# Kernel tuning notes

Measured on AMD Instinct MI355X. Metric: run time of the kernel, lower is better.

Reference implementation:

```python
import jax, jax.numpy as jnp
import numpy as np

K = 9  # kernel_size (knn neighbors, loop=True -> self included)

def setup_inputs() -> dict:
    key = jax.random.key(0)
    k1, k2, k3 = jax.random.split(key, 3)
    B, C, H, W = 8, 64, 32, 32
    OUT = 64
    x = jax.random.normal(k1, (B, C, H, W), dtype=jnp.float32)
    # SAGEConv params: lin_l (neighbor aggregate, with bias), lin_r (root, no bias)
    s = 1.0 / np.sqrt(C)
    W_l = jax.random.uniform(k2, (OUT, C), minval=-s, maxval=s, dtype=jnp.float32)
    b_l = jnp.zeros((OUT,), dtype=jnp.float32)
    W_r = jax.random.uniform(k3, (OUT, C), minval=-s, maxval=s, dtype=jnp.float32)
    return {"x": x, "W_l": W_l, "b_l": b_l, "W_r": W_r}

def _knn_mean(x_f, batches):
    # squared-euclidean pairwise distances [N, N], masked across batches
    sq = jnp.sum(x_f * x_f, axis=-1)
    dist = sq[:, None] + sq[None, :] - 2.0 * (x_f @ x_f.T)
    cross = batches[:, None] != batches[None, :]
    dist = jnp.where(cross, jnp.inf, dist)
    neg, idx = jax.lax.top_k(-dist, K)          # k nearest (self included, dist 0)
    valid = (neg != -jnp.inf).astype(x_f.dtype)  # handle degenerate last-batch node
    nbr = x_f[idx] * valid[..., None]            # [N, K, C]
    return nbr.sum(axis=1) / valid.sum(axis=1, keepdims=True)

def reference(x, W_l, b_l, W_r):
    B, C, H, Wd = x.shape
    N = B * H * Wd
    x_f = x.transpose(0, 2, 3, 1).reshape(N, C)  # flat_nodes: [B*H*W, C]
    # torch.linspace(0, B, steps=N).to(int64): truncation of i*B/(N-1)
    batches = jnp.linspace(0.0, float(B), N).astype(jnp.int32)
    mean_nbr = _knn_mean(x_f, batches)
    # SAGEConv: lin_l(mean_j x_j) + lin_r(x_i)
    return mean_nbr @ W_l.T + b_l + x_f @ W_r.T
```

## Files before the change

kernel.cpp:

```cpp
#include <hip/hip_runtime.h>
#include <cstdint>
#include <cstddef>


__global__ __launch_bounds__(256, 2) void k_dist(const float* __restrict__ x,
                                                 const float* __restrict__ Wl,
                                                 const float* __restrict__ Wr,
                                                 const float* __restrict__ bl,
                                                 float* __restrict__ yl,
                                                 float* __restrict__ yr,
                                                 float* __restrict__ D) {
  __shared__ float4 SH[2112];
  float4* As4 = SH;
  float4* Bs4 = SH + 1056;
  __shared__ float sqA[128];
  __shared__ float sqB[128];
  int bi = (int)blockIdx.x;
  int t = threadIdx.x;
  int tx = t & 15, ty = t >> 4;

  bool is_w = (bi >= 288);
  int i0, j0 = 0, sb = 0, ti = 0, tj = 0;
  if (is_w) {
    i0 = (bi - 288) << 7;
  } else {
    int b = bi / 36;
    int rem = bi - b * 36;
    while (rem >= 8 - ti) { rem -= (8 - ti); ++ti; }
    tj = ti + rem;
    sb = b << 10;
    i0 = sb + (ti << 7);
    j0 = sb + (tj << 7);
  }
  const float* xA = x + (((size_t)(i0 >> 10)) << 16) + (i0 & 1023);
  const float* xB = is_w ? xA : x + (((size_t)(j0 >> 10)) << 16) + (j0 & 1023);

  float acc[8][8];
#pragma unroll
  for (int r = 0; r < 8; ++r)
#pragma unroll
    for (int c = 0; c < 8; ++c) acc[r][c] = 0.f;

#pragma unroll 1
  for (int pass = 0; pass < 2; ++pass) {
    if (pass) __syncthreads();
    int c0 = pass << 5;
#pragma unroll
    for (int i = 0; i < 4; ++i) {
      int u = t + (i << 8);
      int c = u >> 5, m4 = u & 31;
      As4[c * 33 + m4] = *(const float4*)&xA[((size_t)(c0 + c) << 10) + (m4 << 2)];
    }
    if (!is_w) {
#pragma unroll
      for (int i = 0; i < 4; ++i) {
        int u = t + (i << 8);
        int c = u >> 5, m4 = u & 31;
        Bs4[c * 33 + m4] = *(const float4*)&xB[((size_t)(c0 + c) << 10) + (m4 << 2)];
      }
    } else {
#pragma unroll
      for (int i = 0; i < 16; ++i) {
        int u = t + (i << 8);
        int j = u >> 5, c = u & 31;
        const float* Wsrc = (j < 64) ? Wl : Wr;
        int jr = j & 63;
        ((float*)&Bs4[c * 33 + (j >> 2)])[j & 3] = Wsrc[(jr << 6) + c0 + c];
      }
    }
    __syncthreads();
    if (!is_w) {
      int m = t & 127;
      const float* base = (t < 128) ? (const float*)As4 : (const float*)Bs4;
      float p = 0.f;
#pragma unroll
      for (int c = 0; c < 32; ++c) {
        float v = base[(c * 33 + (m >> 2)) * 4 + (m & 3)];
        p = fmaf(v, v, p);
      }
      float* dst = (t < 128) ? sqA : sqB;
      if (pass == 0) dst[m] = p; else dst[m] += p;
    }
#pragma unroll 4
    for (int k = 0; k < 32; ++k) {
      float4 a0 = As4[k * 33 + ty];
      float4 a1 = As4[k * 33 + 16 + ty];
      float4 b0 = Bs4[k * 33 + tx];
      float4 b1 = Bs4[k * 33 + 16 + tx];
      float av[8] = {a0.x, a0.y, a0.z, a0.w, a1.x, a1.y, a1.z, a1.w};
      float bv[8] = {b0.x, b0.y, b0.z, b0.w, b1.x, b1.y, b1.z, b1.w};
#pragma unroll
      for (int r = 0; r < 8; ++r)
#pragma unroll
        for (int c = 0; c < 8; ++c)
          acc[r][c] = fmaf(av[r], bv[c], acc[r][c]);
    }
  }
  __syncthreads();

  int rloc[8];
#pragma unroll
  for (int r = 0; r < 4; ++r) { rloc[r] = (ty << 2) + r; rloc[4 + r] = 64 + (ty << 2) + r; }

  if (is_w) {
    float4 blv = *(const float4*)&bl[tx << 2];
#pragma unroll
    for (int r = 0; r < 8; ++r) {
      int n = i0 + rloc[r];
      float4 o0, o1;
      o0.x = acc[r][0]; o0.y = acc[r][1]; o0.z = acc[r][2]; o0.w = acc[r][3];
      o1.x = acc[r][4] + blv.x; o1.y = acc[r][5] + blv.y;
      o1.z = acc[r][6] + blv.z; o1.w = acc[r][7] + blv.w;
      *(float4*)&yl[((size_t)n << 6) + (tx << 2)] = o0;
      *(float4*)&yr[((size_t)n << 6) + (tx << 2)] = o1;
    }
    return;
  }

  int cloc[8];
#pragma unroll
  for (int c = 0; c < 4; ++c) { cloc[c] = (tx << 2) + c; cloc[4 + c] = 64 + (tx << 2) + c; }
  float sqi[8], sqj[8];
#pragma unroll
  for (int r = 0; r < 8; ++r) sqi[r] = sqA[rloc[r]];
#pragma unroll
  for (int c = 0; c < 8; ++c) sqj[c] = sqB[cloc[c]];
#pragma unroll
  for (int r = 0; r < 8; ++r)
#pragma unroll
    for (int c = 0; c < 8; ++c)
      acc[r][c] = sqi[r] + sqj[c] - 2.f * acc[r][c];
#pragma unroll
  for (int r = 0; r < 8; ++r) {
    size_t rb = ((size_t)(i0 + rloc[r]) << 10) + (j0 - sb);
    float4 o0, o1;
    o0.x = acc[r][0]; o0.y = acc[r][1]; o0.z = acc[r][2]; o0.w = acc[r][3];
    o1.x = acc[r][4]; o1.y = acc[r][5]; o1.z = acc[r][6]; o1.w = acc[r][7];
    *(float4*)&D[rb + (tx << 2)] = o0;
    *(float4*)&D[rb + 64 + (tx << 2)] = o1;
  }
  if (ti != tj) {
    float* tb = (float*)SH;
#pragma unroll 1
    for (int h = 0; h < 2; ++h) {
      __syncthreads();
#pragma unroll
      for (int r = 0; r < 8; ++r)
#pragma unroll
        for (int c = 0; c < 4; ++c)
          tb[((tx << 2) + c) * 132 + rloc[r]] = acc[r][(h << 2) + c];
      __syncthreads();
#pragma unroll
      for (int it = 0; it < 8; ++it) {
        int lin = t + (it << 8);
        int j2 = lin >> 5, u = lin & 31;
        float4 v = *(const float4*)&tb[j2 * 132 + (u << 2)];
        *(float4*)&D[((size_t)(j0 + (h << 6) + j2) << 10) + (i0 - sb) + (u << 2)] = v;
      }
    }
  }
}

__global__ __launch_bounds__(256, 4) void k_selout(const float* __restrict__ D,
                                                   const float* __restrict__ yl,
                                                   const float* __restrict__ yr,
                                                   float* __restrict__ out) {
  int t = threadIdx.x;
  int lane = t & 63;
  int w = t >> 6;
  int n = ((int)blockIdx.x << 2) + w;

  float rv = yr[((size_t)n << 6) + lane];
  float acc;
  if (n == 8191) {
    acc = yl[((size_t)n << 6) + lane];
  } else {
    int s = (n >= 7168) ? 7168 : (n & ~1023);
    bool mlast = (n >= 7168);
    const float* drow = D + ((size_t)n << 10);
    unsigned long long cand[16];
#pragma unroll
    for (int q = 0; q < 4; ++q) {
      float4 v = *(const float4*)&drow[(q << 8) + (lane << 2)];
      float vv[4] = {v.x, v.y, v.z, v.w};
#pragma unroll
      for (int e = 0; e < 4; ++e) {
        unsigned u = __float_as_uint(vv[e]);
        u = (u & 0x80000000u) ? ~u : (u | 0x80000000u);
        unsigned jj = (unsigned)((q << 8) + (lane << 2) + e);
        cand[(q << 2) + e] = ((unsigned long long)u << 32) | jj;
      }
    }
    if (mlast && lane == 63) cand[15] = ~0ull;
    unsigned long long m1 = cand[0], m2 = cand[1];
    if (m2 < m1) { unsigned long long tt = m1; m1 = m2; m2 = tt; }
#pragma unroll
    for (int q = 2; q < 16; ++q) {
      unsigned long long c = cand[q];
      unsigned long long lo = (c < m1) ? c : m1;
      unsigned long long hi = (c < m1) ? m1 : c;
      m2 = (hi < m2) ? hi : m2;
      m1 = lo;
    }
    unsigned long long lm = m1;
    unsigned rmask = 0;
    bool stale = false;
    unsigned j9[9];
#pragma unroll
    for (int kk = 0; kk < 9; ++kk) {
      unsigned long long g = lm;
#pragma unroll
      for (int off = 32; off; off >>= 1) {
        unsigned ghi = __shfl_xor((unsigned)(g >> 32), off, 64);
        unsigned glo = __shfl_xor((unsigned)g, off, 64);
        unsigned long long o = ((unsigned long long)ghi << 32) | glo;
        g = (o < g) ? o : g;
      }
      j9[kk] = (unsigned)s + ((unsigned)g & 1023u);
      if (lm == g) {
        unsigned slot = (((unsigned)g >> 6) & 12u) | ((unsigned)g & 3u);
        rmask |= 1u << slot;
        if (!stale) { lm = m2; stale = true; }
        else {
          unsigned long long best = ~0ull;
#pragma unroll
          for (int q = 0; q < 16; ++q) {
            bool alive = ((rmask >> q) & 1u) == 0u;
            unsigned long long c = cand[q];
            best = (alive && c < best) ? c : best;
          }
          lm = best;
        }
      }
    }
    float g0 = yl[((size_t)j9[0] << 6) + lane];
    float g1 = yl[((size_t)j9[1] << 6) + lane];
    float g2 = yl[((size_t)j9[2] << 6) + lane];
    float g3 = yl[((size_t)j9[3] << 6) + lane];
    float g4 = yl[((size_t)j9[4] << 6) + lane];
    float g5 = yl[((size_t)j9[5] << 6) + lane];
    float g6 = yl[((size_t)j9[6] << 6) + lane];
    float g7 = yl[((size_t)j9[7] << 6) + lane];
    float g8 = yl[((size_t)j9[8] << 6) + lane];
    acc = (((g0 + g1) + (g2 + g3)) + ((g4 + g5) + (g6 + g7)) + g8) * (1.f / 9.f);
  }
  out[((size_t)n << 6) + lane] = acc + rv;
}

extern "C" void kernel_launch(void* const* d_in, const int* in_sizes, int n_in,
                              void* d_out, int out_size, void* d_ws, size_t ws_size,
                              hipStream_t stream) {
  const float* x  = (const float*)d_in[0];
  const float* Wl = (const float*)d_in[1];
  const float* bl = (const float*)d_in[2];
  const float* Wr = (const float*)d_in[3];
  float* out = (float*)d_out;

  char* ws = (char*)d_ws;
  float* yl = (float*)(ws);
  float* yr = (float*)(ws + 2097152);
  float* D  = (float*)(ws + 4194304);

  k_dist<<<dim3(352), 256, 0, stream>>>(x, Wl, Wr, bl, yl, yr, D);
  k_selout<<<2048, 256, 0, stream>>>(D, yl, yr, out);
}
```

Baseline: 112.5 us.

## Fuse distance and selection kernels into one launch with a flag-based grid barrier

```diff
diff --git a/kernel.cpp b/kernel.cpp
--- a/kernel.cpp
+++ b/kernel.cpp
@@ -3,13 +3,17 @@
 #include <cstddef>
 
 
-__global__ __launch_bounds__(256, 2) void k_dist(const float* __restrict__ x,
-                                                 const float* __restrict__ Wl,
-                                                 const float* __restrict__ Wr,
-                                                 const float* __restrict__ bl,
-                                                 float* __restrict__ yl,
-                                                 float* __restrict__ yr,
-                                                 float* __restrict__ D) {
+#define BARRIER_MAGIC 0x1F2E3D4Cu
+
+__global__ __launch_bounds__(256, 2) void k_fused(const float* __restrict__ x,
+                                                  const float* __restrict__ Wl,
+                                                  const float* __restrict__ Wr,
+                                                  const float* __restrict__ bl,
+                                                  float* __restrict__ yl,
+                                                  float* __restrict__ yr,
+                                                  float* __restrict__ D,
+                                                  unsigned* __restrict__ flags,
+                                                  float* __restrict__ out) {
   __shared__ float4 SH[2112];
   float4* As4 = SH;
   float4* Bs4 = SH + 1056;
@@ -19,232 +23,256 @@
   int t = threadIdx.x;
   int tx = t & 15, ty = t >> 4;
 
-  bool is_w = (bi >= 288);
-  int i0, j0 = 0, sb = 0, ti = 0, tj = 0;
-  if (is_w) {
-    i0 = (bi - 288) << 7;
-  } else {
-    int b = bi / 36;
-    int rem = bi - b * 36;
-    while (rem >= 8 - ti) { rem -= (8 - ti); ++ti; }
-    tj = ti + rem;
-    sb = b << 10;
-    i0 = sb + (ti << 7);
-    j0 = sb + (tj << 7);
-  }
-  const float* xA = x + (((size_t)(i0 >> 10)) << 16) + (i0 & 1023);
-  const float* xB = is_w ? xA : x + (((size_t)(j0 >> 10)) << 16) + (j0 & 1023);
-
-  float acc[8][8];
-#pragma unroll
-  for (int r = 0; r < 8; ++r)
-#pragma unroll
-    for (int c = 0; c < 8; ++c) acc[r][c] = 0.f;
+  if (bi < 352) {
+    bool is_w = (bi >= 288);
+    int i0, j0 = 0, sb = 0, ti = 0, tj = 0;
+    if (is_w) {
+      i0 = (bi - 288) << 7;
+    } else {
+      int b = bi / 36;
+      int rem = bi - b * 36;
+      while (rem >= 8 - ti) { rem -= (8 - ti); ++ti; }
+      tj = ti + rem;
+      sb = b << 10;
+      i0 = sb + (ti << 7);
+      j0 = sb + (tj << 7);
+    }
+    const float* xA = x + (((size_t)(i0 >> 10)) << 16) + (i0 & 1023);
+    const float* xB = is_w ? xA : x + (((size_t)(j0 >> 10)) << 16) + (j0 & 1023);
+
+    float acc[8][8];
+#pragma unroll
+    for (int r = 0; r < 8; ++r)
+#pragma unroll
+      for (int c = 0; c < 8; ++c) acc[r][c] = 0.f;
 
 #pragma unroll 1
-  for (int pass = 0; pass < 2; ++pass) {
-    if (pass) __syncthreads();
-    int c0 = pass << 5;
-#pragma unroll
-    for (int i = 0; i < 4; ++i) {
-      int u = t + (i << 8);
-      int c = u >> 5, m4 = u & 31;
-      As4[c * 33 + m4] = *(const float4*)&xA[((size_t)(c0 + c) << 10) + (m4 << 2)];
-    }
-    if (!is_w) {
+    for (int pass = 0; pass < 2; ++pass) {
+      if (pass) __syncthreads();
+      int c0 = pass << 5;
 #pragma unroll
       for (int i = 0; i < 4; ++i) {
         int u = t + (i << 8);
         int c = u >> 5, m4 = u & 31;
-        Bs4[c * 33 + m4] = *(const float4*)&xB[((size_t)(c0 + c) << 10) + (m4 << 2)];
+        As4[c * 33 + m4] = *(const float4*)&xA[((size_t)(c0 + c) << 10) + (m4 << 2)];
+      }
+      if (!is_w) {
+#pragma unroll
+        for (int i = 0; i < 4; ++i) {
+          int u = t + (i << 8);
+          int c = u >> 5, m4 = u & 31;
+          Bs4[c * 33 + m4] = *(const float4*)&xB[((size_t)(c0 + c) << 10) + (m4 << 2)];
+        }
+      } else {
+#pragma unroll
+        for (int i = 0; i < 16; ++i) {
+          int u = t + (i << 8);
+          int j = u >> 5, c = u & 31;
+          const float* Wsrc = (j < 64) ? Wl : Wr;
+          int jr = j & 63;
+          ((float*)&Bs4[c * 33 + (j >> 2)])[j & 3] = Wsrc[(jr << 6) + c0 + c];
+        }
+      }
+      __syncthreads();
+      if (!is_w) {
+        int m = t & 127;
+        const float* base = (t < 128) ? (const float*)As4 : (const float*)Bs4;
+        float p = 0.f;
+#pragma unroll
+        for (int c = 0; c < 32; ++c) {
+          float v = base[(c * 33 + (m >> 2)) * 4 + (m & 3)];
+          p = fmaf(v, v, p);
+        }
+        float* dst = (t < 128) ? sqA : sqB;
+        if (pass == 0) dst[m] = p; else dst[m] += p;
+      }
+#pragma unroll 4
+      for (int k = 0; k < 32; ++k) {
+        float4 a0 = As4[k * 33 + ty];
+        float4 a1 = As4[k * 33 + 16 + ty];
+        float4 b0 = Bs4[k * 33 + tx];
+        float4 b1 = Bs4[k * 33 + 16 + tx];
+        float av[8] = {a0.x, a0.y, a0.z, a0.w, a1.x, a1.y, a1.z, a1.w};
+        float bv[8] = {b0.x, b0.y, b0.z, b0.w, b1.x, b1.y, b1.z, b1.w};
+#pragma unroll
+        for (int r = 0; r < 8; ++r)
+#pragma unroll
+          for (int c = 0; c < 8; ++c)
+            acc[r][c] = fmaf(av[r], bv[c], acc[r][c]);
+      }
+    }
+    __syncthreads();
+
+    int rloc[8];
+#pragma unroll
+    for (int r = 0; r < 4; ++r) { rloc[r] = (ty << 2) + r; rloc[4 + r] = 64 + (ty << 2) + r; }
+
+    if (is_w) {
+      float4 blv = *(const float4*)&bl[tx << 2];
+#pragma unroll
+      for (int r = 0; r < 8; ++r) {
+        int n = i0 + rloc[r];
+        float4 o0, o1;
+        o0.x = acc[r][0]; o0.y = acc[r][1]; o0.z = acc[r][2]; o0.w = acc[r][3];
+        o1.x = acc[r][4] + blv.x; o1.y = acc[r][5] + blv.y;
+        o1.z = acc[r][6] + blv.z; o1.w = acc[r][7] + blv.w;
+        *(float4*)&yl[((size_t)n << 6) + (tx << 2)] = o0;
+        *(float4*)&yr[((size_t)n << 6) + (tx << 2)] = o1;
       }
     } else {
-#pragma unroll
-      for (int i = 0; i < 16; ++i) {
-        int u = t + (i << 8);
-        int j = u >> 5, c = u & 31;
-        const float* Wsrc = (j < 64) ? Wl : Wr;
-        int jr = j & 63;
-        ((float*)&Bs4[c * 33 + (j >> 2)])[j & 3] = Wsrc[(jr << 6) + c0 + c];
+      int cloc[8];
+#pragma unroll
+      for (int c = 0; c < 4; ++c) { cloc[c] = (tx << 2) + c; cloc[4 + c] = 64 + (tx << 2) + c; }
+      float sqi[8], sqj[8];
+#pragma unroll
+      for (int r = 0; r < 8; ++r) sqi[r] = sqA[rloc[r]];
+#pragma unroll
+      for (int c = 0; c < 8; ++c) sqj[c] = sqB[cloc[c]];
+#pragma unroll
+      for (int r = 0; r < 8; ++r)
+#pragma unroll
+        for (int c = 0; c < 8; ++c)
+          acc[r][c] = sqi[r] + sqj[c] - 2.f * acc[r][c];
+#pragma unroll
+      for (int r = 0; r < 8; ++r) {
+        size_t rb = ((size_t)(i0 + rloc[r]) << 10) + (j0 - sb);
+        float4 o0, o1;
+        o0.x = acc[r][0]; o0.y = acc[r][1]; o0.z = acc[r][2]; o0.w = acc[r][3];
+        o1.x = acc[r][4]; o1.y = acc[r][5]; o1.z = acc[r][6]; o1.w = acc[r][7];
+        *(float4*)&D[rb + (tx << 2)] = o0;
+        *(float4*)&D[rb + 64 + (tx << 2)] = o1;
+      }
+      if (ti != tj) {
+        float* tb = (float*)SH;
+#pragma unroll 1
+        for (int h = 0; h < 2; ++h) {
+          __syncthreads();
+#pragma unroll
+          for (int r = 0; r < 8; ++r)
+#pragma unroll
+            for (int c = 0; c < 4; ++c)
+              tb[((tx << 2) + c) * 132 + rloc[r]] = acc[r][(h << 2) + c];
+          __syncthreads();
+#pragma unroll
+          for (int it = 0; it < 8; ++it) {
+            int lin = t + (it << 8);
+            int j2 = lin >> 5, u = lin & 31;
+            float4 v = *(const float4*)&tb[j2 * 132 + (u << 2)];
+            *(float4*)&D[((size_t)(j0 + (h << 6) + j2) << 10) + (i0 - sb) + (u << 2)] = v;
+          }
+        }
       }
     }
     __syncthreads();
-    if (!is_w) {
-      int m = t & 127;
-      const float* base = (t < 128) ? (const float*)As4 : (const float*)Bs4;
-      float p = 0.f;
-#pragma unroll
-      for (int c = 0; c < 32; ++c) {
-        float v = base[(c * 33 + (m >> 2)) * 4 + (m & 3)];
-        p = fmaf(v, v, p);
-      }
-      float* dst = (t < 128) ? sqA : sqB;
-      if (pass == 0) dst[m] = p; else dst[m] += p;
-    }
-#pragma unroll 4
-    for (int k = 0; k < 32; ++k) {
-      float4 a0 = As4[k * 33 + ty];
-      float4 a1 = As4[k * 33 + 16 + ty];
-      float4 b0 = Bs4[k * 33 + tx];
-      float4 b1 = Bs4[k * 33 + 16 + tx];
-      float av[8] = {a0.x, a0.y, a0.z, a0.w, a1.x, a1.y, a1.z, a1.w};
-      float bv[8] = {b0.x, b0.y, b0.z, b0.w, b1.x, b1.y, b1.z, b1.w};
-#pragma unroll
-      for (int r = 0; r < 8; ++r)
-#pragma unroll
-        for (int c = 0; c < 8; ++c)
-          acc[r][c] = fmaf(av[r], bv[c], acc[r][c]);
-    }
+    if (t == 0) {
+      __threadfence();
+      __hip_atomic_store(&flags[bi << 4], BARRIER_MAGIC, __ATOMIC_RELEASE,
+                         __HIP_MEMORY_SCOPE_AGENT);
+    }
+  }
+
+  if (t < 64) {
+    bool done = false;
+    while (!done) {
+      bool ok = true;
+#pragma unroll
+      for (int q = 0; q < 6; ++q) {
+        int idx = t + (q << 6);
+        unsigned v = (idx < 352)
+            ? __hip_atomic_load(&flags[idx << 4], __ATOMIC_ACQUIRE,
+                                __HIP_MEMORY_SCOPE_AGENT)
+            : BARRIER_MAGIC;
+        ok &= (v == BARRIER_MAGIC);
+      }
+      done = __all(ok);
+      if (!done) __builtin_amdgcn_s_sleep(8);
+    }
+    __threadfence();
   }
   __syncthreads();
 
-  int rloc[8];
-#pragma unroll
-  for (int r = 0; r < 4; ++r) { rloc[r] = (ty << 2) + r; rloc[4 + r] = 64 + (ty << 2) + r; }
-
-  if (is_w) {
-    float4 blv = *(const float4*)&bl[tx << 2];
-#pragma unroll
-    for (int r = 0; r < 8; ++r) {
-      int n = i0 + rloc[r];
-      float4 o0, o1;
-      o0.x = acc[r][0]; o0.y = acc[r][1]; o0.z = acc[r][2]; o0.w = acc[r][3];
-      o1.x = acc[r][4] + blv.x; o1.y = acc[r][5] + blv.y;
-      o1.z = acc[r][6] + blv.z; o1.w = acc[r][7] + blv.w;
-      *(float4*)&yl[((size_t)n << 6) + (tx << 2)] = o0;
-      *(float4*)&yr[((size_t)n << 6) + (tx << 2)] = o1;
-    }
-    return;
-  }
-
-  int cloc[8];
-#pragma unroll
-  for (int c = 0; c < 4; ++c) { cloc[c] = (tx << 2) + c; cloc[4 + c] = 64 + (tx << 2) + c; }
-  float sqi[8], sqj[8];
-#pragma unroll
-  for (int r = 0; r < 8; ++r) sqi[r] = sqA[rloc[r]];
-#pragma unroll
-  for (int c = 0; c < 8; ++c) sqj[c] = sqB[cloc[c]];
-#pragma unroll
-  for (int r = 0; r < 8; ++r)
-#pragma unroll
-    for (int c = 0; c < 8; ++c)
-      acc[r][c] = sqi[r] + sqj[c] - 2.f * acc[r][c];
-#pragma unroll
-  for (int r = 0; r < 8; ++r) {
-    size_t rb = ((size_t)(i0 + rloc[r]) << 10) + (j0 - sb);
-    float4 o0, o1;
-    o0.x = acc[r][0]; o0.y = acc[r][1]; o0.z = acc[r][2]; o0.w = acc[r][3];
-    o1.x = acc[r][4]; o1.y = acc[r][5]; o1.z = acc[r][6]; o1.w = acc[r][7];
-    *(float4*)&D[rb + (tx << 2)] = o0;
-    *(float4*)&D[rb + 64 + (tx << 2)] = o1;
-  }
-  if (ti != tj) {
-    float* tb = (float*)SH;
-#pragma unroll 1
-    for (int h = 0; h < 2; ++h) {
-      __syncthreads();
-#pragma unroll
-      for (int r = 0; r < 8; ++r)
-#pragma unroll
-        for (int c = 0; c < 4; ++c)
-          tb[((tx << 2) + c) * 132 + rloc[r]] = acc[r][(h << 2) + c];
-      __syncthreads();
-#pragma unroll
-      for (int it = 0; it < 8; ++it) {
-        int lin = t + (it << 8);
-        int j2 = lin >> 5, u = lin & 31;
-        float4 v = *(const float4*)&tb[j2 * 132 + (u << 2)];
-        *(float4*)&D[((size_t)(j0 + (h << 6) + j2) << 10) + (i0 - sb) + (u << 2)] = v;
-      }
-    }
-  }
-}
-
-__global__ __launch_bounds__(256, 4) void k_selout(const float* __restrict__ D,
-                                                   const float* __restrict__ yl,
-                                                   const float* __restrict__ yr,
-                                                   float* __restrict__ out) {
-  int t = threadIdx.x;
   int lane = t & 63;
   int w = t >> 6;
-  int n = ((int)blockIdx.x << 2) + w;
-
-  float rv = yr[((size_t)n << 6) + lane];
-  float acc;
-  if (n == 8191) {
-    acc = yl[((size_t)n << 6) + lane];
-  } else {
-    int s = (n >= 7168) ? 7168 : (n & ~1023);
-    bool mlast = (n >= 7168);
-    const float* drow = D + ((size_t)n << 10);
-    unsigned long long cand[16];
-#pragma unroll
-    for (int q = 0; q < 4; ++q) {
-      float4 v = *(const float4*)&drow[(q << 8) + (lane << 2)];
-      float vv[4] = {v.x, v.y, v.z, v.w};
-#pragma unroll
-      for (int e = 0; e < 4; ++e) {
-        unsigned u = __float_as_uint(vv[e]);
-        u = (u & 0x80000000u) ? ~u : (u | 0x80000000u);
-        unsigned jj = (unsigned)((q << 8) + (lane << 2) + e);
-        cand[(q << 2) + e] = ((unsigned long long)u << 32) | jj;
-      }
-    }
-    if (mlast && lane == 63) cand[15] = ~0ull;
-    unsigned long long m1 = cand[0], m2 = cand[1];
-    if (m2 < m1) { unsigned long long tt = m1; m1 = m2; m2 = tt; }
-#pragma unroll
-    for (int q = 2; q < 16; ++q) {
-      unsigned long long c = cand[q];
-      unsigned long long lo = (c < m1) ? c : m1;
-      unsigned long long hi = (c < m1) ? m1 : c;
-      m2 = (hi < m2) ? hi : m2;
-      m1 = lo;
-    }
-    unsigned long long lm = m1;
-    unsigned rmask = 0;
-    bool stale = false;
-    unsigned j9[9];
-#pragma unroll
-    for (int kk = 0; kk < 9; ++kk) {
-      unsigned long long g = lm;
-#pragma unroll
-      for (int off = 32; off; off >>= 1) {
-        unsigned ghi = __shfl_xor((unsigned)(g >> 32), off, 64);
-        unsigned glo = __shfl_xor((unsigned)g, off, 64);
-        unsigned long long o = ((unsigned long long)ghi << 32) | glo;
-        g = (o < g) ? o : g;
-      }
-      j9[kk] = (unsigned)s + ((unsigned)g & 1023u);
-      if (lm == g) {
-        unsigned slot = (((unsigned)g >> 6) & 12u) | ((unsigned)g & 3u);
-        rmask |= 1u << slot;
-        if (!stale) { lm = m2; stale = true; }
-        else {
-          unsigned long long best = ~0ull;
-#pragma unroll
-          for (int q = 0; q < 16; ++q) {
-            bool alive = ((rmask >> q) & 1u) == 0u;
-            unsigned long long c = cand[q];
-            best = (alive && c < best) ? c : best;
+  int n0 = (bi << 4) + (w << 2);
+#pragma unroll 1
+  for (int rr = 0; rr < 4; ++rr) {
+    int n = n0 + rr;
+    float rv = yr[((size_t)n << 6) + lane];
+    float accv;
+    if (n == 8191) {
+      accv = yl[((size_t)n << 6) + lane];
+    } else {
+      int s = (n >= 7168) ? 7168 : (n & ~1023);
+      bool mlast = (n >= 7168);
+      const float* drow = D + ((size_t)n << 10);
+      unsigned long long cand[16];
+#pragma unroll
+      for (int q = 0; q < 4; ++q) {
+        float4 v = *(const float4*)&drow[(q << 8) + (lane << 2)];
+        float vv[4] = {v.x, v.y, v.z, v.w};
+#pragma unroll
+        for (int e = 0; e < 4; ++e) {
+          unsigned u = __float_as_uint(vv[e]);
+          u = (u & 0x80000000u) ? ~u : (u | 0x80000000u);
+          unsigned jj = (unsigned)((q << 8) + (lane << 2) + e);
+          cand[(q << 2) + e] = ((unsigned long long)u << 32) | jj;
+        }
+      }
+      if (mlast && lane == 63) cand[15] = ~0ull;
+      unsigned long long m1 = cand[0], m2 = cand[1];
+      if (m2 < m1) { unsigned long long tt = m1; m1 = m2; m2 = tt; }
+#pragma unroll
+      for (int q = 2; q < 16; ++q) {
+        unsigned long long c = cand[q];
+        unsigned long long lo = (c < m1) ? c : m1;
+        unsigned long long hi = (c < m1) ? m1 : c;
+        m2 = (hi < m2) ? hi : m2;
+        m1 = lo;
+      }
+      unsigned long long lm = m1;
+      unsigned rmask = 0;
+      bool stale = false;
+      unsigned j9[9];
+#pragma unroll
+      for (int kk = 0; kk < 9; ++kk) {
+        unsigned long long g = lm;
+#pragma unroll
+        for (int off = 32; off; off >>= 1) {
+          unsigned ghi = __shfl_xor((unsigned)(g >> 32), off, 64);
+          unsigned glo = __shfl_xor((unsigned)g, off, 64);
+          unsigned long long o = ((unsigned long long)ghi << 32) | glo;
+          g = (o < g) ? o : g;
+        }
+        j9[kk] = (unsigned)s + ((unsigned)g & 1023u);
+        if (lm == g) {
+          unsigned slot = (((unsigned)g >> 6) & 12u) | ((unsigned)g & 3u);
+          rmask |= 1u << slot;
+          if (!stale) { lm = m2; stale = true; }
+          else {
+            unsigned long long best = ~0ull;
+#pragma unroll
+            for (int q = 0; q < 16; ++q) {
+              bool alive = ((rmask >> q) & 1u) == 0u;
+              unsigned long long c = cand[q];
+              best = (alive && c < best) ? c : best;
+            }
+            lm = best;
           }
-          lm = best;
-        }
-      }
-    }
-    float g0 = yl[((size_t)j9[0] << 6) + lane];
-    float g1 = yl[((size_t)j9[1] << 6) + lane];
-    float g2 = yl[((size_t)j9[2] << 6) + lane];
-    float g3 = yl[((size_t)j9[3] << 6) + lane];
-    float g4 = yl[((size_t)j9[4] << 6) + lane];
-    float g5 = yl[((size_t)j9[5] << 6) + lane];
-    float g6 = yl[((size_t)j9[6] << 6) + lane];
-    float g7 = yl[((size_t)j9[7] << 6) + lane];
-    float g8 = yl[((size_t)j9[8] << 6) + lane];
-    acc = (((g0 + g1) + (g2 + g3)) + ((g4 + g5) + (g6 + g7)) + g8) * (1.f / 9.f);
+        }
+      }
+      float g0 = yl[((size_t)j9[0] << 6) + lane];
+      float g1 = yl[((size_t)j9[1] << 6) + lane];
+      float g2 = yl[((size_t)j9[2] << 6) + lane];
+      float g3 = yl[((size_t)j9[3] << 6) + lane];
+      float g4 = yl[((size_t)j9[4] << 6) + lane];
+      float g5 = yl[((size_t)j9[5] << 6) + lane];
+      float g6 = yl[((size_t)j9[6] << 6) + lane];
+      float g7 = yl[((size_t)j9[7] << 6) + lane];
+      float g8 = yl[((size_t)j9[8] << 6) + lane];
+      accv = (((g0 + g1) + (g2 + g3)) + ((g4 + g5) + (g6 + g7)) + g8) * (1.f / 9.f);
+    }
+    out[((size_t)n << 6) + lane] = accv + rv;
   }
-  out[((size_t)n << 6) + lane] = acc + rv;
 }
 
 extern "C" void kernel_launch(void* const* d_in, const int* in_sizes, int n_in,
@@ -260,7 +288,7 @@
   float* yl = (float*)(ws);
   float* yr = (float*)(ws + 2097152);
   float* D  = (float*)(ws + 4194304);
-
-  k_dist<<<dim3(352), 256, 0, stream>>>(x, Wl, Wr, bl, yl, yr, D);
-  k_selout<<<2048, 256, 0, stream>>>(D, yl, yr, out);
+  unsigned* flags = (unsigned*)(ws + 37748736);
+
+  k_fused<<<dim3(512), 256, 0, stream>>>(x, Wl, Wr, bl, yl, yr, D, flags, out);
 }
```

Result: slower. 299.3 us (+166.0%).
